# Kernel optimization log

Hardware: AMD Instinct MI355X
Metric: run time of the kernel (lower is better)

## Reference

```python
import jax, jax.numpy as jnp
import numpy as np

N_NODES = 500_000
DIM_IN = 128
DIM_OUT = 128
N_DISTRICTS = 1024


def setup_inputs() -> dict:
    key = jax.random.key(0)
    k_x, k_z, k_w1, k_w2 = jax.random.split(key, 4)
    x = jax.random.normal(k_x, (N_NODES, DIM_IN), dtype=jnp.float32)
    zone_lst = jax.random.randint(k_z, (N_NODES,), 0, N_DISTRICTS, dtype=jnp.int64)
    # MLP params: Linear(dim_in, 2*dim_in), Linear(2*dim_in, dim_out)
    w1 = jax.random.normal(k_w1, (DIM_IN, 2 * DIM_IN), dtype=jnp.float32) * (1.0 / np.sqrt(DIM_IN))
    b1 = jnp.zeros((2 * DIM_IN,), dtype=jnp.float32)
    w2 = jax.random.normal(k_w2, (2 * DIM_IN, DIM_OUT), dtype=jnp.float32) * (1.0 / np.sqrt(2 * DIM_IN))
    b2 = jnp.zeros((DIM_OUT,), dtype=jnp.float32)
    return {"x": x, "zone_lst": zone_lst, "w1": w1, "b1": b1, "w2": w2, "b2": b2}


def reference(x, zone_lst, w1, b1, w2, b2):
    # Per-district sum of node features: one fused segment reduction
    # (replaces the python loop over districts in the original).
    head = jax.ops.segment_sum(x, zone_lst, num_segments=N_DISTRICTS)  # [D, dim_in]
    # MLP: ReLU -> Linear -> ReLU -> Linear
    h = jnp.maximum(head, 0.0)
    h = jnp.maximum(h @ w1 + b1, 0.0)
    return h @ w2 + b2
```

## Files before the change

kernel.cpp:

```cpp
#include <hip/hip_runtime.h>

#define DIM_IN 128
#define DIM_HID 256
#define DIM_OUT 128
#define N_DIST 1024
#define NB 256


__device__ __forceinline__ int detect_is64(const int* __restrict__ zone_raw,
                                           int t, int* s_flag) {
    if (t < 64) {
        bool hi_zero = (zone_raw[2 * t + 1] == 0);
        unsigned long long m = __ballot(hi_zero);
        if (t == 0) *s_flag = (m == ~0ull) ? 1 : 0;
    }
    __syncthreads();
    return *s_flag;
}

__global__ __launch_bounds__(256)
void hist_kernel(const int* __restrict__ zone, int n,
                 int* __restrict__ blockHist) {
    __shared__ int lhist[N_DIST];
    __shared__ int s_is64;
    const int t = threadIdx.x;
    const int b = blockIdx.x;
    for (int i = t; i < N_DIST; i += 256) lhist[i] = 0;
    const int is64 = detect_is64(zone, t, &s_is64);

    const int chunk = (n + NB - 1) / NB;
    const int start = b * chunk;
    const int end = min(n, start + chunk);
    const long long* zone64 = (const long long*)zone;
    for (int i = start + t; i < end; i += 256) {
        int z = is64 ? (int)zone64[i] : zone[i];
        atomicAdd(&lhist[z], 1);
    }
    __syncthreads();
    for (int i = t; i < N_DIST; i += 256) blockHist[b * N_DIST + i] = lhist[i];
}

__global__ __launch_bounds__(256)
void scanA_kernel(int* __restrict__ blockHist, int* __restrict__ counts) {
    const int t = threadIdx.x;
    const int lane = t & 63;
    const int w = t >> 6;
    const int d = blockIdx.x * 4 + w;

    int v0 = blockHist[(4 * lane + 0) * N_DIST + d];
    int v1 = blockHist[(4 * lane + 1) * N_DIST + d];
    int v2 = blockHist[(4 * lane + 2) * N_DIST + d];
    int v3 = blockHist[(4 * lane + 3) * N_DIST + d];
    const int tsum = v0 + v1 + v2 + v3;

    int s = tsum;
#pragma unroll
    for (int off = 1; off < 64; off <<= 1) {
        int u = __shfl_up(s, off);
        if (lane >= off) s += u;
    }
    const int total = __shfl(s, 63);
    int excl = s - tsum;

    blockHist[(4 * lane + 0) * N_DIST + d] = excl; excl += v0;
    blockHist[(4 * lane + 1) * N_DIST + d] = excl; excl += v1;
    blockHist[(4 * lane + 2) * N_DIST + d] = excl; excl += v2;
    blockHist[(4 * lane + 3) * N_DIST + d] = excl;

    if (lane == 0) counts[d] = total;
}

__global__ __launch_bounds__(1024)
void scanB_kernel(const int* __restrict__ counts, int* __restrict__ offsets) {
    __shared__ int tmp[N_DIST];
    const int d = threadIdx.x;
    const int c = counts[d];
    tmp[d] = c;
    __syncthreads();
    for (int off = 1; off < N_DIST; off <<= 1) {
        int add = (d >= off) ? tmp[d - off] : 0;
        __syncthreads();
        tmp[d] += add;
        __syncthreads();
    }
    offsets[d] = tmp[d] - c;
}

__global__ __launch_bounds__(256)
void scatter_kernel(const int* __restrict__ zone, int n,
                    const int* __restrict__ blockStart,
                    const int* __restrict__ offsets,
                    int* __restrict__ sorted) {
    __shared__ int lcur[N_DIST];
    __shared__ int s_is64;
    const int t = threadIdx.x;
    const int b = blockIdx.x;
    for (int i = t; i < N_DIST; i += 256)
        lcur[i] = offsets[i] + blockStart[b * N_DIST + i];
    const int is64 = detect_is64(zone, t, &s_is64);

    const int chunk = (n + NB - 1) / NB;
    const int start = b * chunk;
    const int end = min(n, start + chunk);
    const long long* zone64 = (const long long*)zone;
    for (int i = start + t; i < end; i += 256) {
        int z = is64 ? (int)zone64[i] : zone[i];
        int pos = atomicAdd(&lcur[z], 1);
        sorted[pos] = i;
    }
}

__global__ __launch_bounds__(256)
void district_kernel(const float* __restrict__ x, const int* __restrict__ sorted,
                     const int* __restrict__ offsets, const int* __restrict__ counts,
                     const float* __restrict__ w1, const float* __restrict__ b1,
                     const float* __restrict__ w2, const float* __restrict__ b2,
                     float* __restrict__ out) {
    const int d = blockIdx.x;
    const int start = offsets[d];
    const int cnt = counts[d];
    const int t = threadIdx.x;
    const int q = t & 31;
    const int g = t >> 5;

    __shared__ int sidx[1024];

    const float* xq = x + (size_t)q * 4;
    float4 a0 = make_float4(0.f, 0.f, 0.f, 0.f);
    float4 a1 = a0, a2 = a0, a3 = a0;

    for (int base = 0; base < cnt; base += 1024) {
        const int m = min(cnt - base, 1024);
        for (int i = t; i < m; i += 256) sidx[i] = sorted[start + base + i];
        __syncthreads();

        int n = g;
        for (; n + 24 < m; n += 32) {
            int i0 = sidx[n];
            int i1 = sidx[n + 8];
            int i2 = sidx[n + 16];
            int i3 = sidx[n + 24];
            float4 v0 = *(const float4*)(xq + (size_t)i0 * DIM_IN);
            float4 v1 = *(const float4*)(xq + (size_t)i1 * DIM_IN);
            float4 v2 = *(const float4*)(xq + (size_t)i2 * DIM_IN);
            float4 v3 = *(const float4*)(xq + (size_t)i3 * DIM_IN);
            a0.x += v0.x; a0.y += v0.y; a0.z += v0.z; a0.w += v0.w;
            a1.x += v1.x; a1.y += v1.y; a1.z += v1.z; a1.w += v1.w;
            a2.x += v2.x; a2.y += v2.y; a2.z += v2.z; a2.w += v2.w;
            a3.x += v3.x; a3.y += v3.y; a3.z += v3.z; a3.w += v3.w;
        }
        for (; n < m; n += 8) {
            int i0 = sidx[n];
            float4 v0 = *(const float4*)(xq + (size_t)i0 * DIM_IN);
            a0.x += v0.x; a0.y += v0.y; a0.z += v0.z; a0.w += v0.w;
        }
        __syncthreads();
    }

    a0.x += a1.x + a2.x + a3.x;
    a0.y += a1.y + a2.y + a3.y;
    a0.z += a1.z + a2.z + a3.z;
    a0.w += a1.w + a2.w + a3.w;

    __shared__ float part[8][DIM_IN];
    part[g][q * 4 + 0] = a0.x;
    part[g][q * 4 + 1] = a0.y;
    part[g][q * 4 + 2] = a0.z;
    part[g][q * 4 + 3] = a0.w;
    __syncthreads();

    __shared__ float hrelu[DIM_IN];
    if (t < DIM_IN) {
        float s = 0.f;
#pragma unroll
        for (int gg = 0; gg < 8; gg++) s += part[gg][t];
        hrelu[t] = fmaxf(s, 0.f);
    }
    __syncthreads();

    float s1 = b1[t];
#pragma unroll 8
    for (int k = 0; k < DIM_IN; k++) {
        s1 = fmaf(hrelu[k], w1[k * DIM_HID + t], s1);
    }
    __shared__ float h1[DIM_HID];
    h1[t] = fmaxf(s1, 0.f);
    __syncthreads();

    if (t < DIM_OUT) {
        float s2 = b2[t];
#pragma unroll 8
        for (int j = 0; j < DIM_HID; j++) {
            s2 = fmaf(h1[j], w2[j * DIM_OUT + t], s2);
        }
        out[d * DIM_OUT + t] = s2;
    }
}

extern "C" void kernel_launch(void* const* d_in, const int* in_sizes, int n_in,
                              void* d_out, int out_size, void* d_ws, size_t ws_size,
                              hipStream_t stream) {
    const float* x    = (const float*)d_in[0];
    const int*   zone = (const int*)d_in[1];
    const float* w1   = (const float*)d_in[2];
    const float* b1   = (const float*)d_in[3];
    const float* w2   = (const float*)d_in[4];
    const float* b2   = (const float*)d_in[5];
    float* out = (float*)d_out;
    const int n = in_sizes[0] / DIM_IN;

    char* ws = (char*)d_ws;
    int* counts    = (int*)(ws);
    int* offsets   = (int*)(ws + 4096);
    int* blockHist = (int*)(ws + 65536);
    int* sorted    = (int*)(ws + (2u << 20));

    hist_kernel<<<NB, 256, 0, stream>>>(zone, n, blockHist);
    scanA_kernel<<<N_DIST / 4, 256, 0, stream>>>(blockHist, counts);
    scanB_kernel<<<1, N_DIST, 0, stream>>>(counts, offsets);
    scatter_kernel<<<NB, 256, 0, stream>>>(zone, n, blockHist, offsets, sorted);
    district_kernel<<<N_DIST, 256, 0, stream>>>(x, sorted, offsets, counts,
                                                w1, b1, w2, b2, out);
}
```

Measured before the change: 388.4 us.

## Fold district offset scan into scatter kernel and widen district blocks

Removes the single-block scanB kernel: every scatter block now recomputes the exclusive prefix over the 1024 district counts with wave shuffles and shared memory, and block 0 writes the offsets out for later use. The district kernel doubles its block to 512 threads, giving 16 row groups gathering node features. The two MLP layers are split along K across thread halves and quarters, with partial sums reduced in shared memory. This cuts a launch and a serial scan and adds memory-level parallelism in the gather, at the cost of redundant scan work in each block and more shared memory per block.

```diff
diff --git a/kernel.cpp b/kernel.cpp
--- a/kernel.cpp
+++ b/kernel.cpp
@@ -70,33 +70,46 @@
     if (lane == 0) counts[d] = total;
 }
 
-__global__ __launch_bounds__(1024)
-void scanB_kernel(const int* __restrict__ counts, int* __restrict__ offsets) {
-    __shared__ int tmp[N_DIST];
-    const int d = threadIdx.x;
-    const int c = counts[d];
-    tmp[d] = c;
-    __syncthreads();
-    for (int off = 1; off < N_DIST; off <<= 1) {
-        int add = (d >= off) ? tmp[d - off] : 0;
-        __syncthreads();
-        tmp[d] += add;
-        __syncthreads();
-    }
-    offsets[d] = tmp[d] - c;
-}
-
 __global__ __launch_bounds__(256)
 void scatter_kernel(const int* __restrict__ zone, int n,
                     const int* __restrict__ blockStart,
-                    const int* __restrict__ offsets,
+                    const int* __restrict__ counts,
+                    int* __restrict__ offsets,
                     int* __restrict__ sorted) {
+    __shared__ int off[N_DIST];
     __shared__ int lcur[N_DIST];
+    __shared__ int wsum[4];
     __shared__ int s_is64;
     const int t = threadIdx.x;
     const int b = blockIdx.x;
+    const int lane = t & 63;
+    const int w = t >> 6;
+
+    int4 c4 = ((const int4*)counts)[t];
+    const int tsum = c4.x + c4.y + c4.z + c4.w;
+    int s = tsum;
+#pragma unroll
+    for (int o = 1; o < 64; o <<= 1) {
+        int u = __shfl_up(s, o);
+        if (lane >= o) s += u;
+    }
+    if (lane == 63) wsum[w] = s;
+    __syncthreads();
+    int wbase = 0;
+#pragma unroll
+    for (int ww = 0; ww < 3; ww++) wbase += (ww < w) ? wsum[ww] : 0;
+    int excl = wbase + s - tsum;
+    off[4 * t + 0] = excl;
+    off[4 * t + 1] = excl + c4.x;
+    off[4 * t + 2] = excl + c4.x + c4.y;
+    off[4 * t + 3] = excl + c4.x + c4.y + c4.z;
+    __syncthreads();
+
     for (int i = t; i < N_DIST; i += 256)
-        lcur[i] = offsets[i] + blockStart[b * N_DIST + i];
+        lcur[i] = off[i] + blockStart[b * N_DIST + i];
+    if (b == 0)
+        for (int i = t; i < N_DIST; i += 256) offsets[i] = off[i];
+
     const int is64 = detect_is64(zone, t, &s_is64);
 
     const int chunk = (n + NB - 1) / NB;
@@ -110,7 +123,8 @@
     }
 }
 
-__global__ __launch_bounds__(256)
+#define NG 16
+__global__ __launch_bounds__(512)
 void district_kernel(const float* __restrict__ x, const int* __restrict__ sorted,
                      const int* __restrict__ offsets, const int* __restrict__ counts,
                      const float* __restrict__ w1, const float* __restrict__ b1,
@@ -131,15 +145,15 @@
 
     for (int base = 0; base < cnt; base += 1024) {
         const int m = min(cnt - base, 1024);
-        for (int i = t; i < m; i += 256) sidx[i] = sorted[start + base + i];
+        for (int i = t; i < m; i += 512) sidx[i] = sorted[start + base + i];
         __syncthreads();
 
         int n = g;
-        for (; n + 24 < m; n += 32) {
+        for (; n + 3 * NG < m; n += 4 * NG) {
             int i0 = sidx[n];
-            int i1 = sidx[n + 8];
-            int i2 = sidx[n + 16];
-            int i3 = sidx[n + 24];
+            int i1 = sidx[n + NG];
+            int i2 = sidx[n + 2 * NG];
+            int i3 = sidx[n + 3 * NG];
             float4 v0 = *(const float4*)(xq + (size_t)i0 * DIM_IN);
             float4 v1 = *(const float4*)(xq + (size_t)i1 * DIM_IN);
             float4 v2 = *(const float4*)(xq + (size_t)i2 * DIM_IN);
@@ -149,7 +163,7 @@
             a2.x += v2.x; a2.y += v2.y; a2.z += v2.z; a2.w += v2.w;
             a3.x += v3.x; a3.y += v3.y; a3.z += v3.z; a3.w += v3.w;
         }
-        for (; n < m; n += 8) {
+        for (; n < m; n += NG) {
             int i0 = sidx[n];
             float4 v0 = *(const float4*)(xq + (size_t)i0 * DIM_IN);
             a0.x += v0.x; a0.y += v0.y; a0.z += v0.z; a0.w += v0.w;
@@ -162,7 +176,7 @@
     a0.z += a1.z + a2.z + a3.z;
     a0.w += a1.w + a2.w + a3.w;
 
-    __shared__ float part[8][DIM_IN];
+    __shared__ float part[NG][DIM_IN];
     part[g][q * 4 + 0] = a0.x;
     part[g][q * 4 + 1] = a0.y;
     part[g][q * 4 + 2] = a0.z;
@@ -173,27 +187,41 @@
     if (t < DIM_IN) {
         float s = 0.f;
 #pragma unroll
-        for (int gg = 0; gg < 8; gg++) s += part[gg][t];
+        for (int gg = 0; gg < NG; gg++) s += part[gg][t];
         hrelu[t] = fmaxf(s, 0.f);
     }
     __syncthreads();
 
-    float s1 = b1[t];
+    {
+        const int c = t & 255;
+        const int h = t >> 8;
+        float s1 = 0.f;
+        const int k0 = h * 64;
 #pragma unroll 8
-    for (int k = 0; k < DIM_IN; k++) {
-        s1 = fmaf(hrelu[k], w1[k * DIM_HID + t], s1);
-    }
-    __shared__ float h1[DIM_HID];
-    h1[t] = fmaxf(s1, 0.f);
-    __syncthreads();
-
-    if (t < DIM_OUT) {
-        float s2 = b2[t];
+        for (int k = k0; k < k0 + 64; k++) {
+            s1 = fmaf(hrelu[k], w1[k * DIM_HID + c], s1);
+        }
+        __shared__ float p1[2][DIM_HID];
+        p1[h][c] = s1;
+        __syncthreads();
+        __shared__ float h1s[DIM_HID];
+        if (t < DIM_HID) h1s[t] = fmaxf(b1[t] + p1[0][t] + p1[1][t], 0.f);
+        __syncthreads();
+
+        const int c2 = t & 127;
+        const int hh = t >> 7;
+        float s2 = 0.f;
+        const int j0 = hh * 64;
 #pragma unroll 8
-        for (int j = 0; j < DIM_HID; j++) {
-            s2 = fmaf(h1[j], w2[j * DIM_OUT + t], s2);
-        }
-        out[d * DIM_OUT + t] = s2;
+        for (int j = j0; j < j0 + 64; j++) {
+            s2 = fmaf(h1s[j], w2[j * DIM_OUT + c2], s2);
+        }
+        __shared__ float p2[4][DIM_OUT];
+        p2[hh][c2] = s2;
+        __syncthreads();
+        if (t < DIM_OUT)
+            out[d * DIM_OUT + t] =
+                b2[t] + p2[0][t] + p2[1][t] + p2[2][t] + p2[3][t];
     }
 }
 
@@ -217,8 +245,8 @@
 
     hist_kernel<<<NB, 256, 0, stream>>>(zone, n, blockHist);
     scanA_kernel<<<N_DIST / 4, 256, 0, stream>>>(blockHist, counts);
-    scanB_kernel<<<1, N_DIST, 0, stream>>>(counts, offsets);
-    scatter_kernel<<<NB, 256, 0, stream>>>(zone, n, blockHist, offsets, sorted);
-    district_kernel<<<N_DIST, 256, 0, stream>>>(x, sorted, offsets, counts,
+    scatter_kernel<<<NB, 256, 0, stream>>>(zone, n, blockHist, counts,
+                                           offsets, sorted);
+    district_kernel<<<N_DIST, 512, 0, stream>>>(x, sorted, offsets, counts,
                                                 w1, b1, w2, b2, out);
 }
```

Result: no change. 382.6 us (-1.5%).
